# Kernel optimization log

Hardware: AMD Instinct MI355X
Metric: run time of the kernel (lower is better)

## Reference

```python
import jax, jax.numpy as jnp
import numpy as np

NV = [12544, 6272, 3136, 1568, 784]  # vertex counts, fine -> coarse
SPIRAL = 9


def _grid_sample(im, grid):
    """Faithful port of the hand-rolled bilinear_grid_sample, align_corners=True.
    im: (n, c, h, w); grid: (n, gh, gw, 2) in [-1, 1]. Returns (n, c, gh*gw)."""
    n, c, h, w = im.shape
    gx = grid[..., 0].reshape(n, -1)
    gy = grid[..., 1].reshape(n, -1)
    x = (gx + 1) / 2 * (w - 1)
    y = (gy + 1) / 2 * (h - 1)
    x0 = jnp.floor(x); y0 = jnp.floor(y)
    x1 = x0 + 1; y1 = y0 + 1
    wa = (x1 - x) * (y1 - y)
    wb = (x1 - x) * (y - y0)
    wc = (x - x0) * (y1 - y)
    wd = (x - x0) * (y - y0)
    imp = jnp.pad(im, ((0, 0), (0, 0), (1, 1), (1, 1)))  # explicit zero pad as in source
    ph, pw = h + 2, w + 2
    x0i = jnp.clip(x0.astype(jnp.int32) + 1, 0, pw - 1)
    x1i = jnp.clip(x1.astype(jnp.int32) + 1, 0, pw - 1)
    y0i = jnp.clip(y0.astype(jnp.int32) + 1, 0, ph - 1)
    y1i = jnp.clip(y1.astype(jnp.int32) + 1, 0, ph - 1)
    impf = imp.reshape(n, c, -1)

    def gat(xi, yi):
        idx = xi + yi * pw  # (n, P)
        return jnp.take_along_axis(impf, idx[:, None, :], axis=2)  # (n, c, P)

    Ia = gat(x0i, y0i); Ib = gat(x0i, y1i); Ic = gat(x1i, y0i); Id = gat(x1i, y1i)
    return Ia * wa[:, None] + Ib * wb[:, None] + Ic * wc[:, None] + Id * wd[:, None]


def _pool(x, col, val):
    """Mesh up-pooling: gather columns, weight, and 3-way sum per output vertex.
    With row = repeat(arange(n_out), 3) the row_map built in __init__ is exactly
    arange(3*n_out).reshape(n_out, 3), so the three gathers reduce to reshape+sum."""
    out = x[:, col, :] * val[None, :, None]  # (B, 3*n_out, C)
    n_out = val.shape[0] // 3
    return out.reshape(x.shape[0], n_out, 3, x.shape[2]).sum(axis=2)


def _dsconv(x, idx, dw, pw):
    """Depthwise-separable spiral conv: gather spiral neighborhood, depthwise
    conv over spiral dim (per-channel), then 1x1 pointwise projection."""
    gsp = x[:, idx, :]                        # (B, N, S, Cin)
    y = jnp.einsum('bnsc,cs->bnc', gsp, dw)   # depthwise over spiral
    return y @ pw                             # (B, N, Cout)


def setup_inputs() -> dict:
    key = jax.random.key(0)
    ks = jax.random.split(key, 32)
    d = {}
    d['uv'] = jax.random.uniform(ks[0], (16, 64, 2), jnp.float32)
    d['feat'] = jax.random.normal(ks[1], (16, 256, 4, 4), jnp.float32)
    d['upsample'] = jax.random.normal(ks[2], (NV[4], 64), jnp.float32) * 0.01
    chs = [(256, 256), (256, 256), (256, 128), (128, 64)]
    for i, (ci, co) in enumerate(chs):
        d['dw%d' % i] = jax.random.normal(ks[3 + 2 * i], (ci, SPIRAL), jnp.float32) * (1.0 / SPIRAL)
        d['pw%d' % i] = jax.random.normal(ks[4 + 2 * i], (ci, co), jnp.float32) * (ci ** -0.5)
    d['dw_head'] = jax.random.normal(ks[11], (64, SPIRAL), jnp.float32) * (1.0 / SPIRAL)
    d['pw_head'] = jax.random.normal(ks[12], (64, 3), jnp.float32) * (64 ** -0.5)
    for j in range(4):
        n_out, n_in = NV[j], NV[j + 1]
        d['sp_idx_%d' % j] = jax.random.randint(ks[13 + j], (NV[j], SPIRAL), 0, NV[j], dtype=jnp.int32)
        d['up_col_%d' % j] = jax.random.randint(ks[17 + j], (3 * n_out,), 0, n_in, dtype=jnp.int32)
        d['up_val_%d' % j] = jax.random.uniform(ks[21 + j], (3 * n_out,), jnp.float32)
    return d


def reference(uv, feat, upsample, dw0, pw0, dw1, pw1, dw2, pw2, dw3, pw3, dw_head, pw_head,
              up_val_0, up_val_1, up_val_2, up_val_3,
              sp_idx_0, sp_idx_1, sp_idx_2, sp_idx_3,
              up_col_0, up_col_1, up_col_2, up_col_3):
    g = jnp.clip((uv - 0.5) * 2.0, -1.0, 1.0)[:, :, None, :]  # (B, P, 1, 2)
    x = _grid_sample(feat, g)            # (B, 256, P)
    x = x.transpose(0, 2, 1)             # (B, P, 256)
    x = jnp.einsum('vp,bpc->bvc', upsample, x)  # (B, 784, 256) coarse mesh feats
    specs = [(up_col_3, up_val_3, sp_idx_3, dw0, pw0),
             (up_col_2, up_val_2, sp_idx_2, dw1, pw1),
             (up_col_1, up_val_1, sp_idx_1, dw2, pw2),
             (up_col_0, up_val_0, sp_idx_0, dw3, pw3)]
    for col, val, idx, dw, pw in specs:
        x = _pool(x, col, val)
        x = jax.nn.relu(_dsconv(x, idx, dw, pw))
    return _dsconv(x, sp_idx_0, dw_head, pw_head)  # (B, 12544, 3)
```

## Files before the change

kernel.cpp:

```cpp
#include <hip/hip_runtime.h>


typedef _Float16 half8 __attribute__((ext_vector_type(8)));
typedef float    f32x4 __attribute__((ext_vector_type(4)));

__device__ __forceinline__ float4 ld4(const float* p) { return *(const float4*)p; }

__device__ __forceinline__ float lo16f(unsigned u) {
  _Float16 h; unsigned short s = (unsigned short)(u & 0xffffu);
  __builtin_memcpy(&h, &s, 2); return (float)h;
}
__device__ __forceinline__ float hi16f(unsigned u) {
  _Float16 h; unsigned short s = (unsigned short)(u >> 16);
  __builtin_memcpy(&h, &s, 2); return (float)h;
}
__device__ __forceinline__ float h2f(unsigned short s) {
  _Float16 h; __builtin_memcpy(&h, &s, 2); return (float)h;
}
__device__ __forceinline__ unsigned short hbits(float v) {
  _Float16 h = (_Float16)v; unsigned short u; __builtin_memcpy(&u, &h, 2); return u;
}
__device__ __forceinline__ unsigned pk2h(float a, float b) {
  return (unsigned)hbits(a) | ((unsigned)hbits(b) << 16);
}
__device__ __forceinline__ void split2h(float v, unsigned short& h, unsigned short& l) {
  _Float16 hf = (_Float16)v;
  float hif = (float)hf;
  _Float16 lf = (_Float16)((v - hif) * 2048.0f);
  __builtin_memcpy(&h, &hf, 2); __builtin_memcpy(&l, &lf, 2);
}
__device__ __forceinline__ void gload_lds16(const unsigned short* g, unsigned short* l) {
  __builtin_amdgcn_global_load_lds(
      (const __attribute__((address_space(1))) unsigned int*)g,
      (__attribute__((address_space(3))) unsigned int*)l, 16, 0, 0);
}

__global__ __launch_bounds__(256) void k_prep_all(
    const float* __restrict__ pw0, const float* __restrict__ pw1,
    const float* __restrict__ pw2, const float* __restrict__ pw3,
    const float* __restrict__ dwh, const float* __restrict__ pwh,
    const float* __restrict__ dw0, const float* __restrict__ dw1,
    const float* __restrict__ dw2, const float* __restrict__ dw3,
    unsigned short* __restrict__ dstPw, unsigned short* __restrict__ dstHead,
    float* __restrict__ dstDw)
{
  const int blk = blockIdx.x, t = threadIdx.x;
  if (blk < 672) {
    const int b = blk;
    const float* src; int ci_sh, co, f, off;
    if (b < 256)      { src = pw0; ci_sh = 8; co = 256; f = b*256 + t;       off = 0; }
    else if (b < 512) { src = pw1; ci_sh = 8; co = 256; f = (b-256)*256 + t; off = 65536; }
    else if (b < 640) { src = pw2; ci_sh = 8; co = 128; f = (b-512)*256 + t; off = 131072; }
    else              { src = pw3; ci_sh = 7; co = 64;  f = (b-640)*256 + t; off = 163840; }
    const int n = f >> ci_sh, k = f & ((1 << ci_sh) - 1);
    float v = src[(size_t)k*co + n];
    unsigned short h, l; split2h(v, h, l);
    dstPw[off + f]          = h;
    dstPw[172032 + off + f] = l;
  } else if (blk < 680) {
    const int i = (blk - 672)*256 + t;
    const int n = i >> 6, c = i & 63;
    float v = 0.f;
    if (n < 27) v = dwh[c*9 + n/3] * pwh[c*3 + n%3];
    unsigned short h, l; split2h(v, h, l);
    dstHead[i] = h; dstHead[2048 + i] = l;
  } else {
    const int i = (blk - 680)*256 + t;
    if (i >= 8064) return;
    const float* src; int rel, C, off;
    if (i < 2304)      { src = dw0; rel = i;        C = 256; off = 0; }
    else if (i < 4608) { src = dw1; rel = i - 2304; C = 256; off = 2304; }
    else if (i < 6912) { src = dw2; rel = i - 4608; C = 256; off = 4608; }
    else               { src = dw3; rel = i - 6912; C = 128; off = 6912; }
    const int s = rel / C, c = rel % C;
    dstDw[off + rel] = src[c*9 + s];
  }
}

__global__ __launch_bounds__(256) void k_samp(
    const float* __restrict__ uv, const float* __restrict__ feat,
    unsigned short* __restrict__ xs)
{
  __shared__ float feat_l[256][17];
  const int tid = threadIdx.x;
  const int b   = blockIdx.x;

  const float* fr = feat + ((size_t)b*256 + tid)*16;
  #pragma unroll
  for (int i = 0; i < 16; i += 4) {
    float4 f = ld4(fr + i);
    feat_l[tid][i+0] = f.x; feat_l[tid][i+1] = f.y;
    feat_l[tid][i+2] = f.z; feat_l[tid][i+3] = f.w;
  }
  #pragma unroll 4
  for (int p = 0; p < 64; ++p) {
    float gx = uv[((size_t)b*64 + p)*2 + 0];
    float gy = uv[((size_t)b*64 + p)*2 + 1];
    gx = fminf(fmaxf((gx - 0.5f)*2.f, -1.f), 1.f);
    gy = fminf(fmaxf((gy - 0.5f)*2.f, -1.f), 1.f);
    float x = (gx + 1.f)*0.5f*3.f;
    float y = (gy + 1.f)*0.5f*3.f;
    float fx = floorf(x), fy = floorf(y);
    int ix0 = (int)fx, iy0 = (int)fy;
    float wx = x - fx, wy = y - fy;
    int ix1 = ix0 + 1 > 3 ? 3 : ix0 + 1;
    int iy1 = iy0 + 1 > 3 ? 3 : iy0 + 1;
    float v00 = feat_l[tid][iy0*4+ix0];
    float v01 = feat_l[tid][iy0*4+ix1];
    float v10 = feat_l[tid][iy1*4+ix0];
    float v11 = feat_l[tid][iy1*4+ix1];
    float xv = (1.f-wy)*((1.f-wx)*v00 + wx*v01) + wy*((1.f-wx)*v10 + wx*v11);
    xs[((size_t)b*64 + p)*256 + tid] = hbits(xv);
  }
}

__global__ __launch_bounds__(256) void k_up(
    const unsigned short* __restrict__ xs, const float* __restrict__ up,
    unsigned short* __restrict__ x0)
{
  const int tid = threadIdx.x;
  const int b   = blockIdx.y;
  const int v0  = blockIdx.x * 16;

  float acc[16];
  #pragma unroll
  for (int i = 0; i < 16; ++i) acc[i] = 0.f;

  #pragma unroll 8
  for (int p = 0; p < 64; ++p) {
    const float xv = h2f(xs[((size_t)b*64 + p)*256 + tid]);
    #pragma unroll
    for (int i = 0; i < 16; ++i)
      acc[i] += up[(size_t)(v0+i)*64 + p] * xv;
  }
  #pragma unroll
  for (int i = 0; i < 16; ++i)
    x0[((size_t)b*784 + v0 + i)*256 + tid] = hbits(acc[i]);
}

template<int C>
__global__ __launch_bounds__(256) void k_pool(
    const unsigned short* __restrict__ x, const int* __restrict__ col,
    const float* __restrict__ val, unsigned short* __restrict__ out,
    int Vin, int Vout)
{
  constexpr int KGc = C/8;
  constexpr int UPB = 2*KGc;
  const int bp = blockIdx.x & 7;
  const int v0 = (blockIdx.x >> 3) * 8;
  const int t  = threadIdx.x;

  #pragma unroll
  for (int i = 0; i < (8*UPB)/256; ++i) {
    const int id = t + i*256;
    const int vl = id / UPB;
    const int rem = id - vl*UPB;
    const int bl = rem / KGc;
    const int kg = rem - bl*KGc;
    const int v  = v0 + vl;
    const int b  = 2*bp + bl;
    const int c0 = col[3*v+0], c1 = col[3*v+1], c2 = col[3*v+2];
    const float w0 = val[3*v+0], w1 = val[3*v+1], w2 = val[3*v+2];
    const uint4 A = *(const uint4*)(x + ((size_t)b*Vin + c0)*C + 8*kg);
    const uint4 B = *(const uint4*)(x + ((size_t)b*Vin + c1)*C + 8*kg);
    const uint4 Cv= *(const uint4*)(x + ((size_t)b*Vin + c2)*C + 8*kg);
    uint4 R;
    R.x = pk2h(w0*lo16f(A.x)+w1*lo16f(B.x)+w2*lo16f(Cv.x),
               w0*hi16f(A.x)+w1*hi16f(B.x)+w2*hi16f(Cv.x));
    R.y = pk2h(w0*lo16f(A.y)+w1*lo16f(B.y)+w2*lo16f(Cv.y),
               w0*hi16f(A.y)+w1*hi16f(B.y)+w2*hi16f(Cv.y));
    R.z = pk2h(w0*lo16f(A.z)+w1*lo16f(B.z)+w2*lo16f(Cv.z),
               w0*hi16f(A.z)+w1*hi16f(B.z)+w2*hi16f(Cv.z));
    R.w = pk2h(w0*lo16f(A.w)+w1*lo16f(B.w)+w2*lo16f(Cv.w),
               w0*hi16f(A.w)+w1*hi16f(B.w)+w2*hi16f(Cv.w));
    *(uint4*)(out + ((size_t)b*Vout + v)*C + 8*kg) = R;
  }
}

template<int CI>
__global__ __launch_bounds__(256) void k_dw(
    const unsigned short* __restrict__ pin, const int* __restrict__ idx,
    const float* __restrict__ dwT, unsigned short* __restrict__ aout,
    int Vin, int VG)
{
  constexpr int KG    = CI/8;
  constexpr int SLOTS = 256/KG;
  constexpr int VPB   = 2*SLOTS;

  const int t     = threadIdx.x;
  const int xcd   = blockIdx.x & 7;
  const int i     = blockIdx.x >> 3;
  const int phase = (i >= VG) ? 1 : 0;
  const int vg    = i - phase*VG;
  const int b     = xcd + 8*phase;
  const int kg    = t & (KG - 1);
  const int slot  = t / KG;
  const int va    = vg*VPB + slot;
  const int vb2   = va + SLOTS;

  const unsigned short* base = pin + (size_t)b*Vin*CI + 8*kg;
  float y0[8], y1[8];
  #pragma unroll
  for (int j = 0; j < 8; ++j) { y0[j] = 0.f; y1[j] = 0.f; }

  #pragma unroll
  for (int s = 0; s < 9; ++s) {
    const float4 wa = *(const float4*)(dwT + s*CI + 8*kg);
    const float4 wb = *(const float4*)(dwT + s*CI + 8*kg + 4);
    const uint4 g0 = *(const uint4*)(base + (size_t)idx[va *9 + s]*CI);
    const uint4 g1 = *(const uint4*)(base + (size_t)idx[vb2*9 + s]*CI);
    y0[0] += wa.x*lo16f(g0.x); y0[1] += wa.y*hi16f(g0.x);
    y0[2] += wa.z*lo16f(g0.y); y0[3] += wa.w*hi16f(g0.y);
    y0[4] += wb.x*lo16f(g0.z); y0[5] += wb.y*hi16f(g0.z);
    y0[6] += wb.z*lo16f(g0.w); y0[7] += wb.w*hi16f(g0.w);
    y1[0] += wa.x*lo16f(g1.x); y1[1] += wa.y*hi16f(g1.x);
    y1[2] += wa.z*lo16f(g1.y); y1[3] += wa.w*hi16f(g1.y);
    y1[4] += wb.x*lo16f(g1.z); y1[5] += wb.y*hi16f(g1.z);
    y1[6] += wb.z*lo16f(g1.w); y1[7] += wb.w*hi16f(g1.w);
  }
  uint4 p0, p1;
  p0.x = pk2h(y0[0], y0[1]); p0.y = pk2h(y0[2], y0[3]);
  p0.z = pk2h(y0[4], y0[5]); p0.w = pk2h(y0[6], y0[7]);
  p1.x = pk2h(y1[0], y1[1]); p1.y = pk2h(y1[2], y1[3]);
  p1.z = pk2h(y1[4], y1[5]); p1.w = pk2h(y1[6], y1[7]);
  *(uint4*)(aout + (size_t)(va *16 + b)*CI + 8*kg) = p0;
  *(uint4*)(aout + (size_t)(vb2*16 + b)*CI + 8*kg) = p1;
}

template<int CI, int COT, int NTW, int NSLICE, bool RELU>
__global__ __launch_bounds__(256) void k_gemm(
    const unsigned short* __restrict__ A,
    const unsigned short* __restrict__ bhp, const unsigned short* __restrict__ blp,
    unsigned short* __restrict__ out, int Vout, int T)
{
  constexpr int CHUNKS = CI/32;
  constexpr int NCOL   = NTW*64;
  constexpr int OROW   = NCOL + 8;
  constexpr int ABYTES = 64*CI*2;
  constexpr int SLOTS  = ABYTES/16;
  constexpr int AUS    = SLOTS*8;
  constexpr int NB     = (NSLICE == 1) ? 2 : 1;

  __shared__ __align__(16) unsigned short a_l[NB*AUS];
  __shared__ __align__(16) unsigned short epi[(NSLICE==2) ? 64*OROW : 1];

  const int t = threadIdx.x;
  const int w = t >> 6, l = t & 15, q = (t >> 4) & 3;
  const int lane6 = t & 63;
  const int tix0 = blockIdx.x * T;
  const int coB  = blockIdx.y * NCOL * NSLICE;

  auto stage = [&](int tix, int sel) {
    const size_t m0 = (size_t)tix * 64;
    unsigned short* dst = a_l + (size_t)sel*AUS;
    #pragma unroll
    for (int r = 0; r < SLOTS/256; ++r) {
      const int s    = t + r*256;
      const int c    = s >> 8;
      const int mt   = (s >> 6) & 3;
      const int ql   = s & 63;
      const int m    = mt*16 + (ql & 15);
      const int koff = c*32 + (ql >> 4)*8;
      gload_lds16(A + (m0 + m)*CI + koff, dst + (size_t)s*8);
    }
  };

  if constexpr (NSLICE == 1) {
    stage(tix0, 0);
    __syncthreads();
    for (int j = 0; j < T; ++j) {
      const int tix = tix0 + j;
      const int sel = j & 1;
      if (j + 1 < T) stage(tix + 1, sel ^ 1);

      const unsigned short* ab = a_l + (size_t)sel*AUS;
      f32x4 ah[4][NTW], ax[4][NTW];
      #pragma unroll
      for (int mt = 0; mt < 4; ++mt)
        #pragma unroll
        for (int n = 0; n < NTW; ++n)
          #pragma unroll
          for (int r = 0; r < 4; ++r) { ah[mt][n][r] = 0.f; ax[mt][n][r] = 0.f; }

      #pragma unroll
      for (int c = 0; c < CHUNKS; ++c) {
        const int k0 = c*32 + q*8;
        half8 fa[4], fbh[NTW], fbl[NTW];
        #pragma unroll
        for (int mt = 0; mt < 4; ++mt)
          fa[mt] = *(const half8*)(ab + (size_t)(c*256 + mt*64 + lane6)*8);
        #pragma unroll
        for (int n = 0; n < NTW; ++n) {
          const size_t boff = (size_t)(coB + (w*NTW + n)*16 + l)*CI + k0;
          fbh[n] = *(const half8*)(bhp + boff);
          fbl[n] = *(const half8*)(blp + boff);
        }
        #pragma unroll
        for (int mt = 0; mt < 4; ++mt)
          #pragma unroll
          for (int n = 0; n < NTW; ++n) {
            ah[mt][n] = __builtin_amdgcn_mfma_f32_16x16x32_f16(fa[mt], fbh[n], ah[mt][n], 0, 0, 0);
            ax[mt][n] = __builtin_amdgcn_mfma_f32_16x16x32_f16(fa[mt], fbl[n], ax[mt][n], 0, 0, 0);
          }
      }

      __syncthreads();
      unsigned short (*ot)[OROW] = (unsigned short (*)[OROW])(a_l + (size_t)sel*AUS);
      #pragma unroll
      for (int mt = 0; mt < 4; ++mt)
        #pragma unroll
        for (int n = 0; n < NTW; ++n) {
          const int colg = (w*NTW + n)*16 + l;
          #pragma unroll
          for (int r = 0; r < 4; ++r) {
            const int row = mt*16 + q*4 + r;
            float v = ah[mt][n][r] + ax[mt][n][r] * (1.0f/2048.0f);
            if (RELU) v = fmaxf(v, 0.f);
            ot[row][colg] = hbits(v);
          }
        }
      __syncthreads();
      constexpr int PR = NCOL/8;
      const size_t m0 = (size_t)tix * 64;
      #pragma unroll
      for (int i = 0; i < (64*PR)/256; ++i) {
        const int item = t + i*256;
        const int r  = item / PR;
        const int cp = (item % PR)*8;
        const size_t m = m0 + r;
        const int v = (int)(m >> 4), b = (int)(m & 15);
        *(uint4*)(out + ((size_t)b*Vout + v)*COT + coB + cp) = *(const uint4*)&ot[r][cp];
      }
      __syncthreads();
    }
  } else {
    unsigned short (*ot)[OROW] = (unsigned short (*)[OROW])&epi[0];
    for (int j = 0; j < T; ++j) {
      const int tix = tix0 + j;
      stage(tix, 0);
      __syncthreads();
      #pragma unroll 1
      for (int sl = 0; sl < 2; ++sl) {
        const int co0 = coB + sl*NCOL;
        f32x4 ah[4][NTW], ax[4][NTW];
        #pragma unroll
        for (int mt = 0; mt < 4; ++mt)
          #pragma unroll
          for (int n = 0; n < NTW; ++n)
            #pragma unroll
            for (int r = 0; r < 4; ++r) { ah[mt][n][r] = 0.f; ax[mt][n][r] = 0.f; }

        #pragma unroll
        for (int c = 0; c < CHUNKS; ++c) {
          const int k0 = c*32 + q*8;
          half8 fa[4], fbh[NTW], fbl[NTW];
          #pragma unroll
          for (int mt = 0; mt < 4; ++mt)
            fa[mt] = *(const half8*)(a_l + (size_t)(c*256 + mt*64 + lane6)*8);
          #pragma unroll
          for (int n = 0; n < NTW; ++n) {
            const size_t boff = (size_t)(co0 + (w*NTW + n)*16 + l)*CI + k0;
            fbh[n] = *(const half8*)(bhp + boff);
            fbl[n] = *(const half8*)(blp + boff);
          }
          #pragma unroll
          for (int mt = 0; mt < 4; ++mt)
            #pragma unroll
            for (int n = 0; n < NTW; ++n) {
              ah[mt][n] = __builtin_amdgcn_mfma_f32_16x16x32_f16(fa[mt], fbh[n], ah[mt][n], 0, 0, 0);
              ax[mt][n] = __builtin_amdgcn_mfma_f32_16x16x32_f16(fa[mt], fbl[n], ax[mt][n], 0, 0, 0);
            }
        }

        __syncthreads();
        #pragma unroll
        for (int mt = 0; mt < 4; ++mt)
          #pragma unroll
          for (int n = 0; n < NTW; ++n) {
            const int colg = (w*NTW + n)*16 + l;
            #pragma unroll
            for (int r = 0; r < 4; ++r) {
              const int row = mt*16 + q*4 + r;
              float v = ah[mt][n][r] + ax[mt][n][r] * (1.0f/2048.0f);
              if (RELU) v = fmaxf(v, 0.f);
              ot[row][colg] = hbits(v);
            }
          }
        __syncthreads();
        constexpr int PR = NCOL/8;
        const size_t m0 = (size_t)tix * 64;
        #pragma unroll
        for (int i = 0; i < (64*PR)/256; ++i) {
          const int item = t + i*256;
          const int r  = item / PR;
          const int cp = (item % PR)*8;
          const size_t m = m0 + r;
          const int v = (int)(m >> 4), b = (int)(m & 15);
          *(uint4*)(out + ((size_t)b*Vout + v)*COT + co0 + cp) = *(const uint4*)&ot[r][cp];
        }
      }
      __syncthreads();
    }
  }
}

__global__ __launch_bounds__(256) void k_gemm_head(
    const unsigned short* __restrict__ A,
    const unsigned short* __restrict__ bhp, const unsigned short* __restrict__ blp,
    const unsigned short* __restrict__ bhT, const unsigned short* __restrict__ blT,
    float* __restrict__ z, int T)
{
  constexpr int CI     = 128;
  constexpr int CHUNKS = 4;
  constexpr int OROW   = 80;
  constexpr int ABYTES = 64*CI*2;
  constexpr int SLOTS  = ABYTES/16;
  constexpr int AUS    = SLOTS*8;

  __shared__ __align__(16) unsigned short a_l[2*AUS];
  __shared__ float zt[4][32][16];

  const int t = threadIdx.x;
  const int w = t >> 6, l = t & 15, q = (t >> 4) & 3;
  const int lane6 = t & 63;
  const int tix0 = blockIdx.x * T;

  auto stage = [&](int tix, int sel) {
    const size_t m0 = (size_t)tix * 64;
    unsigned short* dst = a_l + (size_t)sel*AUS;
    #pragma unroll
    for (int r = 0; r < SLOTS/256; ++r) {
      const int s    = t + r*256;
      const int c    = s >> 8;
      const int mt   = (s >> 6) & 3;
      const int ql   = s & 63;
      const int m    = mt*16 + (ql & 15);
      const int koff = c*32 + (ql >> 4)*8;
      gload_lds16(A + (m0 + m)*CI + koff, dst + (size_t)s*8);
    }
  };

  stage(tix0, 0);
  __syncthreads();
  for (int j = 0; j < T; ++j) {
    const int tix = tix0 + j;
    const int sel = j & 1;
    if (j + 1 < T) stage(tix + 1, sel ^ 1);

    const unsigned short* ab = a_l + (size_t)sel*AUS;
    f32x4 ah[4], ax[4];
    #pragma unroll
    for (int mt = 0; mt < 4; ++mt)
      #pragma unroll
      for (int r = 0; r < 4; ++r) { ah[mt][r] = 0.f; ax[mt][r] = 0.f; }

    #pragma unroll
    for (int c = 0; c < CHUNKS; ++c) {
      const int k0 = c*32 + q*8;
      half8 fa[4];
      #pragma unroll
      for (int mt = 0; mt < 4; ++mt)
        fa[mt] = *(const half8*)(ab + (size_t)(c*256 + mt*64 + lane6)*8);
      const size_t boff = (size_t)(w*16 + l)*CI + k0;
      half8 fbh = *(const half8*)(bhp + boff);
      half8 fbl = *(const half8*)(blp + boff);
      #pragma unroll
      for (int mt = 0; mt < 4; ++mt) {
        ah[mt] = __builtin_amdgcn_mfma_f32_16x16x32_f16(fa[mt], fbh, ah[mt], 0, 0, 0);
        ax[mt] = __builtin_amdgcn_mfma_f32_16x16x32_f16(fa[mt], fbl, ax[mt], 0, 0, 0);
      }
    }

    __syncthreads();
    unsigned short (*ot)[OROW] = (unsigned short (*)[OROW])(a_l + (size_t)sel*AUS);
    #pragma unroll
    for (int mt = 0; mt < 4; ++mt) {
      const int colg = w*16 + l;
      #pragma unroll
      for (int r = 0; r < 4; ++r) {
        const int row = mt*16 + q*4 + r;
        float v = ah[mt][r] + ax[mt][r] * (1.0f/2048.0f);
        ot[row][colg] = hbits(fmaxf(v, 0.f));
      }
    }
    __syncthreads();

    {
      f32x4 acch[2], accl[2];
      #pragma unroll
      for (int n = 0; n < 2; ++n)
        #pragma unroll
        for (int r = 0; r < 4; ++r) { acch[n][r] = 0.f; accl[n][r] = 0.f; }
      #pragma unroll
      for (int c = 0; c < 2; ++c) {
        const int k0 = c*32 + q*8;
        half8 fa = *(const half8*)&ot[w*16 + l][k0];
        #pragma unroll
        for (int n = 0; n < 2; ++n) {
          half8 fbh = *(const half8*)(bhT + (size_t)(n*16 + l)*64 + k0);
          half8 fbl = *(const half8*)(blT + (size_t)(n*16 + l)*64 + k0);
          acch[n] = __builtin_amdgcn_mfma_f32_16x16x32_f16(fa, fbh, acch[n], 0, 0, 0);
          accl[n] = __builtin_amdgcn_mfma_f32_16x16x32_f16(fa, fbl, accl[n], 0, 0, 0);
        }
      }
      #pragma unroll
      for (int n = 0; n < 2; ++n)
        #pragma unroll
        for (int r = 0; r < 4; ++r)
          zt[w][n*16 + l][q*4 + r] = acch[n][r] + accl[n][r] * (1.0f/2048.0f);
    }
    __syncthreads();

    const size_t u0 = (size_t)tix * 4;
    #pragma unroll
    for (int i = 0; i < 7; ++i) {
      const int item = t + i*256;
      if (item < 1728) {
        const int ul  = item / 432;
        const int rem = item - ul*432;
        const int s   = rem / 48;
        const int bj  = rem - s*48;
        const int b   = bj / 3;
        const int jj  = bj - b*3;
        z[(u0 + ul)*432 + rem] = zt[ul][s*3 + jj][b];
      }
    }
    __syncthreads();
  }
}

__global__ __launch_bounds__(256) void k_head2(
    const float* __restrict__ z, const int* __restrict__ idx,
    float* __restrict__ out, int nvert)
{
  const int w    = threadIdx.x >> 6;
  const int lane = threadIdx.x & 63;
  const int v    = blockIdx.x*4 + w;
  if (lane < 48) {
    float acc = 0.f;
    #pragma unroll
    for (int s = 0; s < 9; ++s) {
      const int u = idx[v*9 + s];
      acc += z[(size_t)u*432 + s*48 + lane];
    }
    const int b = lane / 3, j = lane - b*3;
    out[((size_t)b*nvert + v)*3 + j] = acc;
  }
}

extern "C" void kernel_launch(void* const* d_in, const int* in_sizes, int n_in,
                              void* d_out, int out_size, void* d_ws, size_t ws_size,
                              hipStream_t stream)
{
  const float* uv   = (const float*)d_in[0];
  const float* feat = (const float*)d_in[1];
  const float* up   = (const float*)d_in[2];
  const float* dw0  = (const float*)d_in[3];
  const float* pw0  = (const float*)d_in[4];
  const float* dw1  = (const float*)d_in[5];
  const float* pw1  = (const float*)d_in[6];
  const float* dw2  = (const float*)d_in[7];
  const float* pw2  = (const float*)d_in[8];
  const float* dw3  = (const float*)d_in[9];
  const float* pw3  = (const float*)d_in[10];
  const float* dwh  = (const float*)d_in[11];
  const float* pwh  = (const float*)d_in[12];
  const int*   sp0  = (const int*)d_in[13];
  const int*   col0 = (const int*)d_in[14];
  const float* val0 = (const float*)d_in[15];
  const int*   sp1  = (const int*)d_in[16];
  const int*   col1 = (const int*)d_in[17];
  const float* val1 = (const float*)d_in[18];
  const int*   sp2  = (const int*)d_in[19];
  const int*   col2 = (const int*)d_in[20];
  const float* val2 = (const float*)d_in[21];
  const int*   sp3  = (const int*)d_in[22];
  const int*   col3 = (const int*)d_in[23];
  const float* val3 = (const float*)d_in[24];

  unsigned short* bufA  = (unsigned short*)d_ws;
  unsigned short* bufB  = (unsigned short*)((char*)d_ws + 25690112);
  unsigned short* bufC  = (unsigned short*)((char*)d_ws + 77070336);
  unsigned short* pwT   = (unsigned short*)((char*)d_ws + 128450560);
  unsigned short* bhead = (unsigned short*)((char*)d_ws + 129138688);
  float*          dwT   = (float*)((char*)d_ws + 129155072);
  float*          zbuf  = (float*)((char*)d_ws + 129187328);
  unsigned short* xs    = (unsigned short*)((char*)d_ws + 150863360);
  float* outp = (float*)d_out;

  unsigned short* h0 = pwT;            unsigned short* L0 = pwT + 172032;
  unsigned short* h1 = pwT + 65536;    unsigned short* L1 = L0 + 65536;
  unsigned short* h2 = pwT + 131072;   unsigned short* L2 = L0 + 131072;
  unsigned short* h3 = pwT + 163840;   unsigned short* L3 = L0 + 163840;
  unsigned short* hh = bhead;          unsigned short* Lh = bhead + 2048;
  float* dwT0 = dwT;          float* dwT1 = dwT + 2304;
  float* dwT2 = dwT + 4608;   float* dwT3 = dwT + 6912;

  k_prep_all<<<712, 256, 0, stream>>>(pw0, pw1, pw2, pw3, dwh, pwh,
                                      dw0, dw1, dw2, dw3, pwT, bhead, dwT);
  k_samp<<<16, 256, 0, stream>>>(uv, feat, xs);
  k_up<<<dim3(49,16,1), 256, 0, stream>>>(xs, up, bufA);

  k_pool<256><<<1568, 256, 0, stream>>>(bufA, col3, val3, bufB, 784, 1568);
  k_dw<256><<<16*98, 256, 0, stream>>>(bufB, sp3, dwT0, bufC, 1568, 98);
  k_gemm<256,256,2,2,true><<<dim3(196,1), 256, 0, stream>>>(bufC, h0, L0, bufA, 1568, 2);

  k_pool<256><<<3136, 256, 0, stream>>>(bufA, col2, val2, bufB, 1568, 3136);
  k_dw<256><<<16*196, 256, 0, stream>>>(bufB, sp2, dwT1, bufC, 3136, 196);
  k_gemm<256,256,2,2,true><<<dim3(392,1), 256, 0, stream>>>(bufC, h1, L1, bufA, 3136, 2);

  k_pool<256><<<6272, 256, 0, stream>>>(bufA, col1, val1, bufB, 3136, 6272);
  k_dw<256><<<16*392, 256, 0, stream>>>(bufB, sp1, dwT2, bufC, 6272, 392);
  k_gemm<256,128,2,1,true><<<dim3(392,1), 256, 0, stream>>>(bufC, h2, L2, bufA, 6272, 4);

  k_pool<128><<<12544, 256, 0, stream>>>(bufA, col0, val0, bufB, 6272, 12544);
  k_dw<128><<<16*392, 256, 0, stream>>>(bufB, sp0, dwT3, bufC, 12544, 392);
  k_gemm_head<<<dim3(784,1), 256, 0, stream>>>(bufC, h3, L3, hh, Lh, zbuf, 4);

  k_head2<<<3136, 256, 0, stream>>>(zbuf, sp0, outp, 12544);
}
```

Measured before the change: 402.9 us.

## Fuse mesh up-pooling into depthwise spiral gather via precomputed composed indices

Removes the separate pooling kernels and the pooled intermediate buffer. A new prep kernel composes the spiral indices with the pool column and weight tables into 27 entries per output vertex. The depthwise kernel then gathers three source rows per spiral tap and combines them with packed fp16 math. This avoids writing and re-reading the pooled activations, but it triples the gathered loads, since pooled rows are recomputed per spiral neighbour, and it does the weighted sum in fp16 instead of fp32.

```diff
diff --git a/kernel.cpp b/kernel.cpp
--- a/kernel.cpp
+++ b/kernel.cpp
@@ -2,6 +2,7 @@
 
 
 typedef _Float16 half8 __attribute__((ext_vector_type(8)));
+typedef _Float16 h2    __attribute__((ext_vector_type(2)));
 typedef float    f32x4 __attribute__((ext_vector_type(4)));
 
 __device__ __forceinline__ float4 ld4(const float* p) { return *(const float4*)p; }
@@ -23,6 +24,8 @@
 __device__ __forceinline__ unsigned pk2h(float a, float b) {
   return (unsigned)hbits(a) | ((unsigned)hbits(b) << 16);
 }
+__device__ __forceinline__ h2 uash2(unsigned u) { h2 r; __builtin_memcpy(&r, &u, 4); return r; }
+__device__ __forceinline__ unsigned h2asu(h2 h) { unsigned u; __builtin_memcpy(&u, &h, 4); return u; }
 __device__ __forceinline__ void split2h(float v, unsigned short& h, unsigned short& l) {
   _Float16 hf = (_Float16)v;
   float hif = (float)hf;
@@ -77,6 +80,27 @@
   }
 }
 
+__global__ __launch_bounds__(256) void k_prep_idx(
+    const int* __restrict__ sp3, const int* __restrict__ col3, const float* __restrict__ val3,
+    const int* __restrict__ sp2, const int* __restrict__ col2, const float* __restrict__ val2,
+    const int* __restrict__ sp1, const int* __restrict__ col1, const float* __restrict__ val1,
+    const int* __restrict__ sp0, const int* __restrict__ col0, const float* __restrict__ val0,
+    int* __restrict__ cidx, float* __restrict__ cval)
+{
+  const int e = blockIdx.x*256 + threadIdx.x;
+  if (e >= 635040) return;
+  const int* sp; const int* col; const float* val; int rel, off;
+  if (e < 42336)       { sp = sp3; col = col3; val = val3; rel = e;          off = 0; }
+  else if (e < 127008) { sp = sp2; col = col2; val = val2; rel = e - 42336;  off = 42336; }
+  else if (e < 296352) { sp = sp1; col = col1; val = val1; rel = e - 127008; off = 127008; }
+  else                 { sp = sp0; col = col0; val = val0; rel = e - 296352; off = 296352; }
+  const int v = rel / 27, j = rel - v*27;
+  const int s = j / 3, k = j - s*3;
+  const int u = sp[v*9 + s];
+  cidx[off + rel] = col[3*u + k];
+  cval[off + rel] = val[3*u + k];
+}
+
 __global__ __launch_bounds__(256) void k_samp(
     const float* __restrict__ uv, const float* __restrict__ feat,
     unsigned short* __restrict__ xs)
@@ -138,50 +162,11 @@
     x0[((size_t)b*784 + v0 + i)*256 + tid] = hbits(acc[i]);
 }
 
-template<int C>
-__global__ __launch_bounds__(256) void k_pool(
-    const unsigned short* __restrict__ x, const int* __restrict__ col,
-    const float* __restrict__ val, unsigned short* __restrict__ out,
-    int Vin, int Vout)
-{
-  constexpr int KGc = C/8;
-  constexpr int UPB = 2*KGc;
-  const int bp = blockIdx.x & 7;
-  const int v0 = (blockIdx.x >> 3) * 8;
-  const int t  = threadIdx.x;
-
-  #pragma unroll
-  for (int i = 0; i < (8*UPB)/256; ++i) {
-    const int id = t + i*256;
-    const int vl = id / UPB;
-    const int rem = id - vl*UPB;
-    const int bl = rem / KGc;
-    const int kg = rem - bl*KGc;
-    const int v  = v0 + vl;
-    const int b  = 2*bp + bl;
-    const int c0 = col[3*v+0], c1 = col[3*v+1], c2 = col[3*v+2];
-    const float w0 = val[3*v+0], w1 = val[3*v+1], w2 = val[3*v+2];
-    const uint4 A = *(const uint4*)(x + ((size_t)b*Vin + c0)*C + 8*kg);
-    const uint4 B = *(const uint4*)(x + ((size_t)b*Vin + c1)*C + 8*kg);
-    const uint4 Cv= *(const uint4*)(x + ((size_t)b*Vin + c2)*C + 8*kg);
-    uint4 R;
-    R.x = pk2h(w0*lo16f(A.x)+w1*lo16f(B.x)+w2*lo16f(Cv.x),
-               w0*hi16f(A.x)+w1*hi16f(B.x)+w2*hi16f(Cv.x));
-    R.y = pk2h(w0*lo16f(A.y)+w1*lo16f(B.y)+w2*lo16f(Cv.y),
-               w0*hi16f(A.y)+w1*hi16f(B.y)+w2*hi16f(Cv.y));
-    R.z = pk2h(w0*lo16f(A.z)+w1*lo16f(B.z)+w2*lo16f(Cv.z),
-               w0*hi16f(A.z)+w1*hi16f(B.z)+w2*hi16f(Cv.z));
-    R.w = pk2h(w0*lo16f(A.w)+w1*lo16f(B.w)+w2*lo16f(Cv.w),
-               w0*hi16f(A.w)+w1*hi16f(B.w)+w2*hi16f(Cv.w));
-    *(uint4*)(out + ((size_t)b*Vout + v)*C + 8*kg) = R;
-  }
-}
-
 template<int CI>
-__global__ __launch_bounds__(256) void k_dw(
-    const unsigned short* __restrict__ pin, const int* __restrict__ idx,
-    const float* __restrict__ dwT, unsigned short* __restrict__ aout,
-    int Vin, int VG)
+__global__ __launch_bounds__(256) void k_pdw(
+    const unsigned short* __restrict__ pin, const int* __restrict__ cidx,
+    const float* __restrict__ cval, const float* __restrict__ dwT,
+    unsigned short* __restrict__ aout, int Vin, int VG)
 {
   constexpr int KG    = CI/8;
   constexpr int SLOTS = 256/KG;
@@ -207,24 +192,34 @@
   for (int s = 0; s < 9; ++s) {
     const float4 wa = *(const float4*)(dwT + s*CI + 8*kg);
     const float4 wb = *(const float4*)(dwT + s*CI + 8*kg + 4);
-    const uint4 g0 = *(const uint4*)(base + (size_t)idx[va *9 + s]*CI);
-    const uint4 g1 = *(const uint4*)(base + (size_t)idx[vb2*9 + s]*CI);
-    y0[0] += wa.x*lo16f(g0.x); y0[1] += wa.y*hi16f(g0.x);
-    y0[2] += wa.z*lo16f(g0.y); y0[3] += wa.w*hi16f(g0.y);
-    y0[4] += wb.x*lo16f(g0.z); y0[5] += wb.y*hi16f(g0.z);
-    y0[6] += wb.z*lo16f(g0.w); y0[7] += wb.w*hi16f(g0.w);
-    y1[0] += wa.x*lo16f(g1.x); y1[1] += wa.y*hi16f(g1.x);
-    y1[2] += wa.z*lo16f(g1.y); y1[3] += wa.w*hi16f(g1.y);
-    y1[4] += wb.x*lo16f(g1.z); y1[5] += wb.y*hi16f(g1.z);
-    y1[6] += wb.z*lo16f(g1.w); y1[7] += wb.w*hi16f(g1.w);
-  }
-  uint4 p0, p1;
-  p0.x = pk2h(y0[0], y0[1]); p0.y = pk2h(y0[2], y0[3]);
-  p0.z = pk2h(y0[4], y0[5]); p0.w = pk2h(y0[6], y0[7]);
-  p1.x = pk2h(y1[0], y1[1]); p1.y = pk2h(y1[2], y1[3]);
-  p1.z = pk2h(y1[4], y1[5]); p1.w = pk2h(y1[6], y1[7]);
-  *(uint4*)(aout + (size_t)(va *16 + b)*CI + 8*kg) = p0;
-  *(uint4*)(aout + (size_t)(vb2*16 + b)*CI + 8*kg) = p1;
+    #pragma unroll
+    for (int hv = 0; hv < 2; ++hv) {
+      const int vv = hv ? vb2 : va;
+      float* y = hv ? y1 : y0;
+      const int o27 = vv*27 + s*3;
+      const int i0 = cidx[o27], i1 = cidx[o27+1], i2 = cidx[o27+2];
+      const _Float16 c0 = (_Float16)cval[o27], c1 = (_Float16)cval[o27+1], c2 = (_Float16)cval[o27+2];
+      const h2 w0 = {c0, c0}, w1 = {c1, c1}, w2 = {c2, c2};
+      const uint4 g0 = *(const uint4*)(base + (size_t)i0*CI);
+      const uint4 g1 = *(const uint4*)(base + (size_t)i1*CI);
+      const uint4 g2 = *(const uint4*)(base + (size_t)i2*CI);
+      unsigned p0 = h2asu(uash2(g0.x)*w0 + uash2(g1.x)*w1 + uash2(g2.x)*w2);
+      unsigned p1 = h2asu(uash2(g0.y)*w0 + uash2(g1.y)*w1 + uash2(g2.y)*w2);
+      unsigned p2 = h2asu(uash2(g0.z)*w0 + uash2(g1.z)*w1 + uash2(g2.z)*w2);
+      unsigned p3 = h2asu(uash2(g0.w)*w0 + uash2(g1.w)*w1 + uash2(g2.w)*w2);
+      y[0] += wa.x*lo16f(p0); y[1] += wa.y*hi16f(p0);
+      y[2] += wa.z*lo16f(p1); y[3] += wa.w*hi16f(p1);
+      y[4] += wb.x*lo16f(p2); y[5] += wb.y*hi16f(p2);
+      y[6] += wb.z*lo16f(p3); y[7] += wb.w*hi16f(p3);
+    }
+  }
+  uint4 q0, q1;
+  q0.x = pk2h(y0[0], y0[1]); q0.y = pk2h(y0[2], y0[3]);
+  q0.z = pk2h(y0[4], y0[5]); q0.w = pk2h(y0[6], y0[7]);
+  q1.x = pk2h(y1[0], y1[1]); q1.y = pk2h(y1[2], y1[3]);
+  q1.z = pk2h(y1[4], y1[5]); q1.w = pk2h(y1[6], y1[7]);
+  *(uint4*)(aout + (size_t)(va *16 + b)*CI + 8*kg) = q0;
+  *(uint4*)(aout + (size_t)(vb2*16 + b)*CI + 8*kg) = q1;
 }
 
 template<int CI, int COT, int NTW, int NSLICE, bool RELU>
@@ -579,7 +574,8 @@
   const float* val3 = (const float*)d_in[24];
 
   unsigned short* bufA  = (unsigned short*)d_ws;
-  unsigned short* bufB  = (unsigned short*)((char*)d_ws + 25690112);
+  int*            cidx  = (int*)((char*)d_ws + 25690112);
+  float*          cval  = (float*)((char*)d_ws + 28230272);
   unsigned short* bufC  = (unsigned short*)((char*)d_ws + 77070336);
   unsigned short* pwT   = (unsigned short*)((char*)d_ws + 128450560);
   unsigned short* bhead = (unsigned short*)((char*)d_ws + 129138688);
@@ -598,23 +594,22 @@
 
   k_prep_all<<<712, 256, 0, stream>>>(pw0, pw1, pw2, pw3, dwh, pwh,
                                       dw0, dw1, dw2, dw3, pwT, bhead, dwT);
+  k_prep_idx<<<2481, 256, 0, stream>>>(sp3, col3, val3, sp2, col2, val2,
+                                       sp1, col1, val1, sp0, col0, val0,
+                                       cidx, cval);
   k_samp<<<16, 256, 0, stream>>>(uv, feat, xs);
   k_up<<<dim3(49,16,1), 256, 0, stream>>>(xs, up, bufA);
 
-  k_pool<256><<<1568, 256, 0, stream>>>(bufA, col3, val3, bufB, 784, 1568);
-  k_dw<256><<<16*98, 256, 0, stream>>>(bufB, sp3, dwT0, bufC, 1568, 98);
+  k_pdw<256><<<16*98, 256, 0, stream>>>(bufA, cidx, cval, dwT0, bufC, 784, 98);
   k_gemm<256,256,2,2,true><<<dim3(196,1), 256, 0, stream>>>(bufC, h0, L0, bufA, 1568, 2);
 
-  k_pool<256><<<3136, 256, 0, stream>>>(bufA, col2, val2, bufB, 1568, 3136);
-  k_dw<256><<<16*196, 256, 0, stream>>>(bufB, sp2, dwT1, bufC, 3136, 196);
+  k_pdw<256><<<16*196, 256, 0, stream>>>(bufA, cidx + 42336, cval + 42336, dwT1, bufC, 1568, 196);
   k_gemm<256,256,2,2,true><<<dim3(392,1), 256, 0, stream>>>(bufC, h1, L1, bufA, 3136, 2);
 
-  k_pool<256><<<6272, 256, 0, stream>>>(bufA, col1, val1, bufB, 3136, 6272);
-  k_dw<256><<<16*392, 256, 0, stream>>>(bufB, sp1, dwT2, bufC, 6272, 392);
+  k_pdw<256><<<16*392, 256, 0, stream>>>(bufA, cidx + 127008, cval + 127008, dwT2, bufC, 3136, 392);
   k_gemm<256,128,2,1,true><<<dim3(392,1), 256, 0, stream>>>(bufC, h2, L2, bufA, 6272, 4);
 
-  k_pool<128><<<12544, 256, 0, stream>>>(bufA, col0, val0, bufB, 6272, 12544);
-  k_dw<128><<<16*392, 256, 0, stream>>>(bufB, sp0, dwT3, bufC, 12544, 392);
+  k_pdw<128><<<16*392, 256, 0, stream>>>(bufA, cidx + 296352, cval + 296352, dwT3, bufC, 6272, 392);
   k_gemm_head<<<dim3(784,1), 256, 0, stream>>>(bufC, h3, L3, hh, Lh, zbuf, 4);
 
   k_head2<<<3136, 256, 0, stream>>>(zbuf, sp0, outp, 12544);
```

Measured after the change: 479.3 us. +19.0%, slower.
